# Optimization experiments

Measured on AMD Instinct MI355X. Metric: run time of the kernel, lower is better.

Reference implementation:

```python
import jax, jax.numpy as jnp
import numpy as np

B, N, C = 8, 4096, 768
H = 12            # num_heads
W = 16            # window_size
S = int(N ** 0.5) # 64, token grid side
HD = C // H       # head_dim = 64
WINDOWS = (S // W) ** 2  # 16
NW = W * W               # 256 tokens per window
SCALE = HD ** -0.5


def _window_perm():
    # same ordering as the torch loop: row-major over window blocks,
    # row-major within each window
    idxs = np.arange(N).reshape(S // W, W, S // W, W)
    perm = idxs.transpose(0, 2, 1, 3).reshape(-1)
    inv_perm = np.argsort(perm)
    return jnp.asarray(perm), jnp.asarray(inv_perm)


def setup_inputs() -> dict:
    key = jax.random.key(0)
    kx, kq, kp, kb = jax.random.split(key, 4)
    x = jax.random.normal(kx, (B, N, C), dtype=jnp.float32)
    # torch nn.Linear weights: [out, in]; qkv_bias=False
    qkv_w = jax.random.normal(kq, (3 * C, C), dtype=jnp.float32) * (C ** -0.5)
    proj_w = jax.random.normal(kp, (C, C), dtype=jnp.float32) * (C ** -0.5)
    proj_b = jax.random.normal(kb, (C,), dtype=jnp.float32) * 0.02
    return {"x": x, "qkv_w": qkv_w, "proj_w": proj_w, "proj_b": proj_b}


def reference(x, qkv_w, proj_w, proj_b):
    perm, inv_perm = _window_perm()
    xp = x[:, perm]                                   # [B, N, C] window-ordered
    qkv = xp @ qkv_w.T                                # [B, N, 3C]
    qkv = qkv.reshape(B, WINDOWS, NW, 3, H, HD)
    qkv = jnp.transpose(qkv, (3, 0, 1, 4, 2, 5))      # [3, B, Wn, H, NW, HD]
    q, k, v = qkv[0], qkv[1], qkv[2]
    attn = jnp.einsum('bwhnd,bwhmd->bwhnm', q, k) * SCALE
    attn = jax.nn.softmax(attn, axis=-1)
    out = jnp.einsum('bwhnm,bwhmd->bwhnd', attn, v)   # [B, Wn, H, NW, HD]
    out = jnp.transpose(out, (0, 1, 3, 2, 4)).reshape(B, N, C)
    out = out[:, inv_perm]                            # scatter back to grid order
    return out @ proj_w.T + proj_b
```

## Files before the change

kernel.cpp:

```cpp
#include <hip/hip_runtime.h>
#include <hip/hip_bf16.h>


using short8  = __attribute__((ext_vector_type(8))) short;
using short4v = __attribute__((ext_vector_type(4))) short;
using floatx4 = __attribute__((ext_vector_type(4))) float;

#define B_    8
#define N_    4096
#define C_    768
#define H_    12
#define HD_   64
#define NW_   256
#define SCALE_ 0.125f
#define QKV_PLANE ((size_t)25165824)

__device__ __forceinline__ float bf2f(unsigned short u) {
  union { unsigned int i; float f; } c; c.i = ((unsigned int)u) << 16; return c.f;
}
__device__ __forceinline__ unsigned short f2bf(float f) {
  unsigned int u = __float_as_uint(f);
  u += 0x7fffu + ((u >> 16) & 1u);
  return (unsigned short)(u >> 16);
}
__device__ __forceinline__ short4v f4bf(floatx4 f) {
  short4v s;
  s[0] = (short)f2bf(f[0]); s[1] = (short)f2bf(f[1]);
  s[2] = (short)f2bf(f[2]); s[3] = (short)f2bf(f[3]);
  return s;
}
__device__ __forceinline__ int perm_n(int w, int t) {
  int rb = w >> 2, cb = w & 3, ri = t >> 4, ci = t & 15;
  return ((rb << 4) + ri) * 64 + (cb << 4) + ci;
}
__device__ __forceinline__ void glds16(const unsigned short* g, short* l) {
  __builtin_amdgcn_global_load_lds(
      (const __attribute__((address_space(1))) unsigned int*)g,
      (__attribute__((address_space(3))) unsigned int*)l, 16, 0, 0);
}

__global__ __launch_bounds__(192) void conv_x(
    const float* __restrict__ x, unsigned short* __restrict__ xb) {
  int row = blockIdx.x;
  int b = row >> 12, p = row & 4095;
  int n = perm_n(p >> 8, p & 255);
  const float* src = x + ((size_t)(b << 12) + (size_t)n) * C_;
  unsigned short* dst = xb + (size_t)row * C_;
  int c = threadIdx.x << 2;
  *(short4v*)(dst + c) = f4bf(*(const floatx4*)(src + c));
}

__global__ __launch_bounds__(192) void conv_w(
    const float* __restrict__ qw, const float* __restrict__ pw,
    unsigned short* __restrict__ wq, unsigned short* __restrict__ wp) {
  int row = blockIdx.x;
  const float* src; unsigned short* dst;
  if (row < 2304) { src = qw + (size_t)row * C_; dst = wq + (size_t)row * C_; }
  else { src = pw + (size_t)(row - 2304) * C_; dst = wp + (size_t)(row - 2304) * C_; }
  int c = threadIdx.x << 2;
  *(short4v*)(dst + c) = f4bf(*(const floatx4*)(src + c));
}

#define GEMM_CORE(Aptr, Bptr)                                                  \
  __shared__ short As[128 * 32];                                               \
  __shared__ short Bs[128 * 32];                                               \
  const int tid  = threadIdx.x;                                                \
  const int id0  = (int)(blockIdx.y * gridDim.x + blockIdx.x);                 \
  const int cpx  = (int)(gridDim.x * gridDim.y) >> 3;                          \
  const int swz  = (id0 & 7) * cpx + (id0 >> 3);                               \
  const int bm   = swz & 255;                                                  \
  const int bn   = swz >> 8;                                                   \
  const int wave = tid >> 6, lane = tid & 63;                                  \
  const int wm   = wave >> 1, wn = wave & 1;                                   \
  const int l15  = lane & 15, quad = lane >> 4;                                \
  const int srow = tid >> 2, skof = (tid & 3) << 3;                            \
  const unsigned short* ga0 = (Aptr) + (size_t)(bm * 128 + srow) * C_ + skof;  \
  const unsigned short* ga1 = ga0 + (size_t)64 * C_;                           \
  const unsigned short* gb0 = (Bptr) + (size_t)(bn * 128 + srow) * C_ + skof;  \
  const unsigned short* gb1 = gb0 + (size_t)64 * C_;                           \
  short* la0 = As + tid * 8;                                                   \
  short* la1 = As + 2048 + tid * 8;                                            \
  short* lb0 = Bs + tid * 8;                                                   \
  short* lb1 = Bs + 2048 + tid * 8;                                            \
  floatx4 acc[4][4];                                                           \
  _Pragma("unroll") for (int i = 0; i < 4; i++)                                \
      _Pragma("unroll") for (int j = 0; j < 4; j++)                            \
          acc[i][j] = {0.f, 0.f, 0.f, 0.f};                                    \
  for (int k0 = 0; k0 < C_; k0 += 32) {                                        \
    glds16(ga0 + k0, la0);                                                     \
    glds16(ga1 + k0, la1);                                                     \
    glds16(gb0 + k0, lb0);                                                     \
    glds16(gb1 + k0, lb1);                                                     \
    __syncthreads();                                                           \
    short8 af[4], bfr[4];                                                      \
    _Pragma("unroll") for (int mi = 0; mi < 4; mi++)                           \
        af[mi] = *(const short8*)&As[(wm * 64 + mi * 16 + l15) * 32 + quad * 8];\
    _Pragma("unroll") for (int ni = 0; ni < 4; ni++)                           \
        bfr[ni] = *(const short8*)&Bs[(wn * 64 + ni * 16 + l15) * 32 + quad * 8];\
    _Pragma("unroll") for (int mi = 0; mi < 4; mi++)                           \
        _Pragma("unroll") for (int ni = 0; ni < 4; ni++)                       \
            acc[mi][ni] = __builtin_amdgcn_mfma_f32_16x16x32_bf16(             \
                af[mi], bfr[ni], acc[mi][ni], 0, 0, 0);                        \
    __syncthreads();                                                           \
  }

__global__ __launch_bounds__(256) void qkv_gemm_bf(
    const unsigned short* __restrict__ a,
    const unsigned short* __restrict__ w,
    unsigned short* __restrict__ qkv) {
  GEMM_CORE(a, w)
  const int which = (bn * 128) / 768;
  const int jbase = bn * 128 - which * 768;
  unsigned short* dst = qkv + (size_t)which * QKV_PLANE;
#pragma unroll
  for (int mi = 0; mi < 4; mi++) {
#pragma unroll
    for (int r = 0; r < 4; r++) {
      int mg = bm * 128 + wm * 64 + mi * 16 + quad * 4 + r;
      int b = mg >> 12, p = mg & 4095;
      int wdx = p >> 8, t = p & 255;
      size_t base = (size_t)((b * 16 + wdx) * 12) * (NW_ * HD_) + (size_t)t * HD_;
#pragma unroll
      for (int ni = 0; ni < 4; ni++) {
        int jj = jbase + wn * 64 + ni * 16 + l15;
        int h = jj >> 6, d = jj & 63;
        dst[base + (size_t)h * (NW_ * HD_) + d] = f2bf(acc[mi][ni][r]);
      }
    }
  }
}

__global__ __launch_bounds__(256) void proj_gemm_bf(
    const unsigned short* __restrict__ a,
    const unsigned short* __restrict__ w,
    const float* __restrict__ bias,
    float* __restrict__ out) {
  GEMM_CORE(a, w)
#pragma unroll
  for (int mi = 0; mi < 4; mi++) {
#pragma unroll
    for (int r = 0; r < 4; r++) {
      int mg = bm * 128 + wm * 64 + mi * 16 + quad * 4 + r;
      size_t rowb = (size_t)mg * C_;
#pragma unroll
      for (int ni = 0; ni < 4; ni++) {
        int jj = bn * 128 + wn * 64 + ni * 16 + l15;
        out[rowb + jj] = acc[mi][ni][r] + bias[jj];
      }
    }
  }
}

__global__ __launch_bounds__(512, 2) void attn_mfma(
    const unsigned short* __restrict__ qkv,
    unsigned short* __restrict__ attn_out) {
  const int bwh = blockIdx.x;
  const int tid = threadIdx.x;
  const int wv = tid >> 6, lane = tid & 63;
  const int l15 = lane & 15, quad = lane >> 4;
  const size_t off = (size_t)bwh * (NW_ * HD_);
  const unsigned short* qb = qkv + off;
  const unsigned short* kb = qkv + QKV_PLANE + off;
  const unsigned short* vb = qkv + 2 * QKV_PLANE + off;

  __shared__ short Ks[64 * 72];
  __shared__ short Vt[64 * 72];
  __shared__ short Ps[8][16 * 72];

  short8 bq[2][2];
#pragma unroll
  for (int c = 0; c < 2; c++) {
    int mc = wv + 8 * c;
#pragma unroll
    for (int kc = 0; kc < 2; kc++)
      bq[c][kc] = *(const short8*)(qb + (mc * 16 + l15) * 64 + kc * 32 + quad * 8);
  }

  floatx4 O[2][4];
#pragma unroll
  for (int c = 0; c < 2; c++)
#pragma unroll
    for (int dt = 0; dt < 4; dt++) O[c][dt] = {0.f, 0.f, 0.f, 0.f};
  float m_run[2] = {-1e30f, -1e30f};
  float l_run[2] = {0.f, 0.f};

  const int sr = tid >> 3;
  const int sc = (tid & 7) << 3;

  for (int t = 0; t < 4; t++) {
    __syncthreads();
    {
      short8 kk8 = *(const short8*)(kb + (t * 64 + sr) * 64 + sc);
      *(short8*)&Ks[sr * 72 + sc] = kk8;
      short8 vv8 = *(const short8*)(vb + (t * 64 + sr) * 64 + sc);
#pragma unroll
      for (int j = 0; j < 8; j++) Vt[(sc + j) * 72 + sr] = vv8[j];
    }
    __syncthreads();

#pragma unroll
    for (int c = 0; c < 2; c++) {
      floatx4 st[4];
#pragma unroll
      for (int nt = 0; nt < 4; nt++) {
        short8 ak0 = *(const short8*)&Ks[(nt * 16 + l15) * 72 + quad * 8];
        short8 ak1 = *(const short8*)&Ks[(nt * 16 + l15) * 72 + 32 + quad * 8];
        floatx4 z = {0.f, 0.f, 0.f, 0.f};
        z = __builtin_amdgcn_mfma_f32_16x16x32_bf16(ak0, bq[c][0], z, 0, 0, 0);
        z = __builtin_amdgcn_mfma_f32_16x16x32_bf16(ak1, bq[c][1], z, 0, 0, 0);
        st[nt] = z;
      }
      float s[16];
      float cmax = -1e30f;
#pragma unroll
      for (int nt = 0; nt < 4; nt++)
#pragma unroll
        for (int r = 0; r < 4; r++) {
          float v = st[nt][r] * SCALE_;
          s[nt * 4 + r] = v;
          cmax = fmaxf(cmax, v);
        }
      cmax = fmaxf(cmax, __shfl_xor(cmax, 16));
      cmax = fmaxf(cmax, __shfl_xor(cmax, 32));
      float nm = fmaxf(m_run[c], cmax);
      float alpha = __expf(m_run[c] - nm);
      m_run[c] = nm;
      float psum = 0.f;
#pragma unroll
      for (int j = 0; j < 16; j++) {
        float p = __expf(s[j] - nm);
        s[j] = p;
        psum += p;
      }
      psum += __shfl_xor(psum, 16);
      psum += __shfl_xor(psum, 32);
      l_run[c] = l_run[c] * alpha + psum;
#pragma unroll
      for (int nt = 0; nt < 4; nt++) {
        short4v pv;
        pv[0] = (short)f2bf(s[nt * 4 + 0]);
        pv[1] = (short)f2bf(s[nt * 4 + 1]);
        pv[2] = (short)f2bf(s[nt * 4 + 2]);
        pv[3] = (short)f2bf(s[nt * 4 + 3]);
        *(short4v*)&Ps[wv][l15 * 72 + nt * 16 + quad * 4] = pv;
      }
      float ar[4];
#pragma unroll
      for (int r = 0; r < 4; r++) ar[r] = __shfl(alpha, quad * 4 + r);
#pragma unroll
      for (int dt = 0; dt < 4; dt++)
#pragma unroll
        for (int r = 0; r < 4; r++) O[c][dt][r] *= ar[r];
#pragma unroll
      for (int kc = 0; kc < 2; kc++) {
        short8 ap = *(const short8*)&Ps[wv][l15 * 72 + kc * 32 + quad * 8];
#pragma unroll
        for (int dt = 0; dt < 4; dt++) {
          short8 bv = *(const short8*)&Vt[(dt * 16 + l15) * 72 + kc * 32 + quad * 8];
          O[c][dt] = __builtin_amdgcn_mfma_f32_16x16x32_bf16(ap, bv, O[c][dt], 0, 0, 0);
        }
      }
    }
  }

  int h = bwh % 12, bw = bwh / 12;
  int b = bw >> 4, wdx = bw & 15;
#pragma unroll
  for (int c = 0; c < 2; c++) {
    float linv = 1.f / l_run[c];
    float lr[4];
#pragma unroll
    for (int r = 0; r < 4; r++) lr[r] = __shfl(linv, quad * 4 + r);
    int mc = wv + 8 * c;
#pragma unroll
    for (int r = 0; r < 4; r++) {
      int q = mc * 16 + quad * 4 + r;
      int n = perm_n(wdx, q);
      unsigned short* op = attn_out + ((size_t)(b * N_ + n)) * C_ + h * HD_;
#pragma unroll
      for (int dt = 0; dt < 4; dt++)
        op[dt * 16 + l15] = f2bf(O[c][dt][r] * lr[r]);
    }
  }
}

__global__ __launch_bounds__(256) void qkv_gemm_f32(
    const float* __restrict__ x,
    const float* __restrict__ w,
    unsigned short* __restrict__ qkv) {
  __shared__ short As[128 * 40];
  __shared__ short Bs[128 * 40];
  const int tid  = threadIdx.x;
  const int bm   = blockIdx.x;
  const int bn   = blockIdx.y;
  const int wave = tid >> 6, lane = tid & 63;
  const int wm   = wave >> 1, wn = wave & 1;
  const int l15  = lane & 15, quad = lane >> 4;
  const int colf  = (tid & 7) << 2;
  const int rbase = tid >> 3;
  size_t aoff[4], boff[4];
#pragma unroll
  for (int i = 0; i < 4; i++) {
    int r = rbase + 32 * i;
    int mg = bm * 128 + r;
    int b = mg >> 12, p = mg & 4095;
    int n = perm_n(p >> 8, p & 255);
    aoff[i] = ((size_t)(b << 12) + (size_t)n) * C_;
    boff[i] = (size_t)(bn * 128 + r) * C_;
  }
  floatx4 acc[4][4];
#pragma unroll
  for (int i = 0; i < 4; i++)
#pragma unroll
    for (int j = 0; j < 4; j++) acc[i][j] = {0.f, 0.f, 0.f, 0.f};
  for (int k0 = 0; k0 < C_; k0 += 32) {
#pragma unroll
    for (int i = 0; i < 4; i++) {
      int r = rbase + 32 * i;
      *(short4v*)&As[r * 40 + colf] = f4bf(*(const floatx4*)(x + aoff[i] + k0 + colf));
      *(short4v*)&Bs[r * 40 + colf] = f4bf(*(const floatx4*)(w + boff[i] + k0 + colf));
    }
    __syncthreads();
    short8 af[4], bfr[4];
#pragma unroll
    for (int mi = 0; mi < 4; mi++)
      af[mi] = *(const short8*)&As[(wm * 64 + mi * 16 + l15) * 40 + quad * 8];
#pragma unroll
    for (int ni = 0; ni < 4; ni++)
      bfr[ni] = *(const short8*)&Bs[(wn * 64 + ni * 16 + l15) * 40 + quad * 8];
#pragma unroll
    for (int mi = 0; mi < 4; mi++)
#pragma unroll
      for (int ni = 0; ni < 4; ni++)
        acc[mi][ni] = __builtin_amdgcn_mfma_f32_16x16x32_bf16(
            af[mi], bfr[ni], acc[mi][ni], 0, 0, 0);
    __syncthreads();
  }
  const int which = (bn * 128) / 768;
  const int jbase = bn * 128 - which * 768;
  unsigned short* dst = qkv + (size_t)which * QKV_PLANE;
#pragma unroll
  for (int mi = 0; mi < 4; mi++) {
#pragma unroll
    for (int r = 0; r < 4; r++) {
      int mg = bm * 128 + wm * 64 + mi * 16 + quad * 4 + r;
      int b = mg >> 12, p = mg & 4095;
      int wdx = p >> 8, t = p & 255;
      size_t base = (size_t)((b * 16 + wdx) * 12) * (NW_ * HD_) + (size_t)t * HD_;
#pragma unroll
      for (int ni = 0; ni < 4; ni++) {
        int jj = jbase + wn * 64 + ni * 16 + l15;
        int h = jj >> 6, d = jj & 63;
        dst[base + (size_t)h * (NW_ * HD_) + d] = f2bf(acc[mi][ni][r]);
      }
    }
  }
}

__global__ __launch_bounds__(256) void proj_gemm_f32(
    const unsigned short* __restrict__ a,
    const float* __restrict__ w,
    const float* __restrict__ bias,
    float* __restrict__ out) {
  __shared__ short As[128 * 40];
  __shared__ short Bs[128 * 40];
  const int tid  = threadIdx.x;
  const int bm   = blockIdx.x;
  const int bn   = blockIdx.y;
  const int wave = tid >> 6, lane = tid & 63;
  const int wm   = wave >> 1, wn = wave & 1;
  const int l15  = lane & 15, quad = lane >> 4;
  const int c0 = tid, c1 = tid + 256;
  const int r0 = c0 >> 2, kc0 = (c0 & 3) << 3;
  const int r1 = c1 >> 2, kc1 = (c1 & 3) << 3;
  const size_t a0 = (size_t)(bm * 128 + r0) * C_;
  const size_t a1 = (size_t)(bm * 128 + r1) * C_;
  const int colf  = (tid & 7) << 2;
  const int rbase = tid >> 3;
  size_t boff[4];
#pragma unroll
  for (int i = 0; i < 4; i++)
    boff[i] = (size_t)(bn * 128 + rbase + 32 * i) * C_;
  floatx4 acc[4][4];
#pragma unroll
  for (int i = 0; i < 4; i++)
#pragma unroll
    for (int j = 0; j < 4; j++) acc[i][j] = {0.f, 0.f, 0.f, 0.f};
  for (int k0 = 0; k0 < C_; k0 += 32) {
    *(short8*)&As[r0 * 40 + kc0] = *(const short8*)(a + a0 + k0 + kc0);
    *(short8*)&As[r1 * 40 + kc1] = *(const short8*)(a + a1 + k0 + kc1);
#pragma unroll
    for (int i = 0; i < 4; i++) {
      int r = rbase + 32 * i;
      *(short4v*)&Bs[r * 40 + colf] = f4bf(*(const floatx4*)(w + boff[i] + k0 + colf));
    }
    __syncthreads();
    short8 af[4], bfr[4];
#pragma unroll
    for (int mi = 0; mi < 4; mi++)
      af[mi] = *(const short8*)&As[(wm * 64 + mi * 16 + l15) * 40 + quad * 8];
#pragma unroll
    for (int ni = 0; ni < 4; ni++)
      bfr[ni] = *(const short8*)&Bs[(wn * 64 + ni * 16 + l15) * 40 + quad * 8];
#pragma unroll
    for (int mi = 0; mi < 4; mi++)
#pragma unroll
      for (int ni = 0; ni < 4; ni++)
        acc[mi][ni] = __builtin_amdgcn_mfma_f32_16x16x32_bf16(
            af[mi], bfr[ni], acc[mi][ni], 0, 0, 0);
    __syncthreads();
  }
#pragma unroll
  for (int mi = 0; mi < 4; mi++) {
#pragma unroll
    for (int r = 0; r < 4; r++) {
      int mg = bm * 128 + wm * 64 + mi * 16 + quad * 4 + r;
      size_t rowb = (size_t)mg * C_;
#pragma unroll
      for (int ni = 0; ni < 4; ni++) {
        int jj = bn * 128 + wn * 64 + ni * 16 + l15;
        out[rowb + jj] = acc[mi][ni][r] + bias[jj];
      }
    }
  }
}

extern "C" void kernel_launch(void* const* d_in, const int* in_sizes, int n_in,
                              void* d_out, int out_size, void* d_ws, size_t ws_size,
                              hipStream_t stream) {
  const float* x  = (const float*)d_in[0];
  const float* qw = (const float*)d_in[1];
  const float* pw = (const float*)d_in[2];
  const float* pb = (const float*)d_in[3];
  float* out = (float*)d_out;
  unsigned short* ws = (unsigned short*)d_ws;

  unsigned short* xb       = ws;
  unsigned short* qkv_buf  = ws + QKV_PLANE;
  unsigned short* attn_buf = ws;
  unsigned short* wb_qkv   = ws + 4 * QKV_PLANE;
  unsigned short* wb_proj  = wb_qkv + (size_t)2304 * 768;

  const size_t need = (4 * QKV_PLANE + (size_t)2304 * 768 + (size_t)768 * 768) * 2;
  if (ws_size >= need) {
    conv_x<<<dim3(B_ * N_), dim3(192), 0, stream>>>(x, xb);
    conv_w<<<dim3(3072), dim3(192), 0, stream>>>(qw, pw, wb_qkv, wb_proj);
    qkv_gemm_bf<<<dim3(256, 18), dim3(256), 0, stream>>>(xb, wb_qkv, qkv_buf);
    attn_mfma<<<dim3(1536), dim3(512), 0, stream>>>(qkv_buf, attn_buf);
    proj_gemm_bf<<<dim3(256, 6), dim3(256), 0, stream>>>(attn_buf, wb_proj, pb, out);
  } else {
    qkv_gemm_f32<<<dim3(256, 18), dim3(256), 0, stream>>>(x, qw, qkv_buf);
    attn_mfma<<<dim3(1536), dim3(512), 0, stream>>>(qkv_buf, attn_buf);
    proj_gemm_f32<<<dim3(256, 6), dim3(256), 0, stream>>>(attn_buf, pw, pb, out);
  }
}
```

Before: 484.4 us.

## Rewrite bf16 GEMMs as 256x256 tiles with double-buffered LDS pipeline

Replaces the 128x128, single-buffered GEMM core used by the QKV and projection GEMMs with a 256x256-tile, 8-wave kernel. It uses 128 KB of double-buffered LDS, XOR-swizzled LDS addressing, and phased async global-to-LDS loads that overlap with MFMA work, with explicit barriers, waitcnt and setprio scheduling. The goal is to hide global load latency, raise data reuse per tile and avoid LDS bank conflicts in the GEMMs. The cost is a larger LDS footprint, fewer blocks in the grid and the removal of the L2-friendly block swizzle, plus fragile hand-tuned synchronization.

```diff
diff --git a/kernel.cpp b/kernel.cpp
--- a/kernel.cpp
+++ b/kernel.cpp
@@ -61,65 +61,113 @@
   *(short4v*)(dst + c) = f4bf(*(const floatx4*)(src + c));
 }
 
-#define GEMM_CORE(Aptr, Bptr)                                                  \
-  __shared__ short As[128 * 32];                                               \
-  __shared__ short Bs[128 * 32];                                               \
+#define LPA 0
+#define LPB 16384
+#define LQA 32768
+#define LQB 49152
+
+#define STAGE8(gp, ldsbase, ksk) {                                             \
+    int kc_ = (ksk) < C_ ? (ksk) : 0;                                          \
+    glds16((gp) + (size_t)arow * C_ + kc_ + (sgran << 3),                      \
+           L + (ldsbase) + tid * 8);                                           \
+    glds16((gp) + (size_t)(arow + 64) * C_ + kc_ + (sgran << 3),               \
+           L + (ldsbase) + 4096 + tid * 8);                                    \
+  }
+
+#define PH8(q, AB, BB, LOADB, STG_STMT, WV) {                                  \
+    if (LOADB) {                                                               \
+      _Pragma("unroll") for (int n = 0; n < 4; n++)                            \
+        _Pragma("unroll") for (int kk = 0; kk < 2; kk++)                       \
+          bq[n][kk] = *(const short8*)&L[(BB) + rdB + n * 1024 +               \
+                                          (((kk * 4 + quad) ^ swq) << 3)];     \
+    }                                                                          \
+    short8 a0k0 = *(const short8*)&L[(AB) + rdA + (2*(q))*1024 +               \
+                                      (((quad) ^ swq) << 3)];                  \
+    short8 a0k1 = *(const short8*)&L[(AB) + rdA + (2*(q))*1024 +               \
+                                      (((4 + quad) ^ swq) << 3)];              \
+    short8 a1k0 = *(const short8*)&L[(AB) + rdA + (2*(q)+1)*1024 +             \
+                                      (((quad) ^ swq) << 3)];                  \
+    short8 a1k1 = *(const short8*)&L[(AB) + rdA + (2*(q)+1)*1024 +             \
+                                      (((4 + quad) ^ swq) << 3)];              \
+    STG_STMT;                                                                  \
+    asm volatile("s_barrier" ::: "memory");                                    \
+    asm volatile("s_waitcnt lgkmcnt(0)" ::: "memory");                         \
+    __builtin_amdgcn_sched_barrier(0);                                         \
+    __builtin_amdgcn_s_setprio(1);                                             \
+    _Pragma("unroll") for (int n = 0; n < 4; n++) {                            \
+      acc[2*(q)][n]   = __builtin_amdgcn_mfma_f32_16x16x32_bf16(               \
+          a0k0, bq[n][0], acc[2*(q)][n], 0, 0, 0);                             \
+      acc[2*(q)+1][n] = __builtin_amdgcn_mfma_f32_16x16x32_bf16(               \
+          a1k0, bq[n][0], acc[2*(q)+1][n], 0, 0, 0);                           \
+      acc[2*(q)][n]   = __builtin_amdgcn_mfma_f32_16x16x32_bf16(               \
+          a0k1, bq[n][1], acc[2*(q)][n], 0, 0, 0);                             \
+      acc[2*(q)+1][n] = __builtin_amdgcn_mfma_f32_16x16x32_bf16(               \
+          a1k1, bq[n][1], acc[2*(q)+1][n], 0, 0, 0);                           \
+    }                                                                          \
+    __builtin_amdgcn_s_setprio(0);                                             \
+    if (WV) { asm volatile("s_waitcnt vmcnt(4)" ::: "memory"); }               \
+    asm volatile("s_barrier" ::: "memory");                                    \
+  }
+
+#define GEMM8_CORE(Aptr, Bptr)                                                 \
+  __shared__ short L[65536];                                                   \
   const int tid  = threadIdx.x;                                                \
-  const int id0  = (int)(blockIdx.y * gridDim.x + blockIdx.x);                 \
-  const int cpx  = (int)(gridDim.x * gridDim.y) >> 3;                          \
-  const int swz  = (id0 & 7) * cpx + (id0 >> 3);                               \
-  const int bm   = swz & 255;                                                  \
-  const int bn   = swz >> 8;                                                   \
+  const int bm   = blockIdx.x;                                                 \
+  const int bn   = blockIdx.y;                                                 \
   const int wave = tid >> 6, lane = tid & 63;                                  \
-  const int wm   = wave >> 1, wn = wave & 1;                                   \
+  const int wm   = wave >> 2, wn = wave & 3;                                   \
   const int l15  = lane & 15, quad = lane >> 4;                                \
-  const int srow = tid >> 2, skof = (tid & 3) << 3;                            \
-  const unsigned short* ga0 = (Aptr) + (size_t)(bm * 128 + srow) * C_ + skof;  \
-  const unsigned short* ga1 = ga0 + (size_t)64 * C_;                           \
-  const unsigned short* gb0 = (Bptr) + (size_t)(bn * 128 + srow) * C_ + skof;  \
-  const unsigned short* gb1 = gb0 + (size_t)64 * C_;                           \
-  short* la0 = As + tid * 8;                                                   \
-  short* la1 = As + 2048 + tid * 8;                                            \
-  short* lb0 = Bs + tid * 8;                                                   \
-  short* lb1 = Bs + 2048 + tid * 8;                                            \
-  floatx4 acc[4][4];                                                           \
-  _Pragma("unroll") for (int i = 0; i < 4; i++)                                \
+  const int swq  = l15 & 7;                                                    \
+  const int sgran = (tid & 7) ^ ((tid >> 3) & 7);                              \
+  const int arow  = tid >> 3;                                                  \
+  const unsigned short* gA = (Aptr) + (size_t)(bm * 256) * C_;                 \
+  const unsigned short* gB = (Bptr) + (size_t)(bn * 256) * C_;                 \
+  const unsigned short* gA1 = gA + (size_t)128 * C_;                           \
+  const unsigned short* gB1 = gB + (size_t)128 * C_;                           \
+  const int rdA = wm * 8192 + l15 * 64;                                        \
+  const int rdB = (wn >> 1) * 8192 + ((wn & 1) * 64 + l15) * 64;               \
+  floatx4 acc[8][4];                                                           \
+  short8 bq[4][2];                                                             \
+  _Pragma("unroll") for (int i = 0; i < 8; i++)                                \
       _Pragma("unroll") for (int j = 0; j < 4; j++)                            \
           acc[i][j] = {0.f, 0.f, 0.f, 0.f};                                    \
-  for (int k0 = 0; k0 < C_; k0 += 32) {                                        \
-    glds16(ga0 + k0, la0);                                                     \
-    glds16(ga1 + k0, la1);                                                     \
-    glds16(gb0 + k0, lb0);                                                     \
-    glds16(gb1 + k0, lb1);                                                     \
-    __syncthreads();                                                           \
-    short8 af[4], bfr[4];                                                      \
-    _Pragma("unroll") for (int mi = 0; mi < 4; mi++)                           \
-        af[mi] = *(const short8*)&As[(wm * 64 + mi * 16 + l15) * 32 + quad * 8];\
-    _Pragma("unroll") for (int ni = 0; ni < 4; ni++)                           \
-        bfr[ni] = *(const short8*)&Bs[(wn * 64 + ni * 16 + l15) * 32 + quad * 8];\
-    _Pragma("unroll") for (int mi = 0; mi < 4; mi++)                           \
-        _Pragma("unroll") for (int ni = 0; ni < 4; ni++)                       \
-            acc[mi][ni] = __builtin_amdgcn_mfma_f32_16x16x32_bf16(             \
-                af[mi], bfr[ni], acc[mi][ni], 0, 0, 0);                        \
-    __syncthreads();                                                           \
-  }
-
-__global__ __launch_bounds__(256) void qkv_gemm_bf(
+                           \
+  STAGE8(gA,  LPA,        0); STAGE8(gA1, LPA + 8192, 0);                      \
+  STAGE8(gB,  LPB,        0); STAGE8(gB1, LPB + 8192, 0);                      \
+  STAGE8(gB,  LQB,       64); STAGE8(gB1, LQB + 8192, 64);                     \
+  asm volatile("s_waitcnt vmcnt(4)" ::: "memory");                             \
+  asm volatile("s_barrier" ::: "memory");                                      \
+  for (int it = 0; it < 6; it++) {                                             \
+    const int t  = it * 2;                                                     \
+    const int kA1 = (t + 1) * 64;                                              \
+    const int kN2 = (t + 2) * 64;                                              \
+    const int kN3 = (t + 3) * 64;                                              \
+    PH8(0, LPA, LPB, 1, STAGE8(gA,  LQA,        kA1), 0)                       \
+    PH8(1, LPA, LPB, 0, STAGE8(gA1, LQA + 8192, kA1), 0)                       \
+    PH8(2, LPA, LPB, 0, STAGE8(gB,  LPB,        kN2), 0)                       \
+    PH8(3, LPA, LPB, 0, STAGE8(gB1, LPB + 8192, kN2), 1)                       \
+    PH8(0, LQA, LQB, 1, STAGE8(gA,  LPA,        kN2), 0)                       \
+    PH8(1, LQA, LQB, 0, STAGE8(gA1, LPA + 8192, kN2), 0)                       \
+    PH8(2, LQA, LQB, 0, STAGE8(gB,  LQB,        kN3), 0)                       \
+    PH8(3, LQA, LQB, 0, STAGE8(gB1, LQB + 8192, kN3), 1)                       \
+  }
+
+__global__ __launch_bounds__(512, 2) void qkv_gemm_bf8(
     const unsigned short* __restrict__ a,
     const unsigned short* __restrict__ w,
     unsigned short* __restrict__ qkv) {
-  GEMM_CORE(a, w)
-  const int which = (bn * 128) / 768;
-  const int jbase = bn * 128 - which * 768;
+  GEMM8_CORE(a, w)
+  const int which = bn / 3;
+  const int jbase = (bn - which * 3) * 256;
   unsigned short* dst = qkv + (size_t)which * QKV_PLANE;
 #pragma unroll
-  for (int mi = 0; mi < 4; mi++) {
+  for (int mi = 0; mi < 8; mi++) {
 #pragma unroll
     for (int r = 0; r < 4; r++) {
-      int mg = bm * 128 + wm * 64 + mi * 16 + quad * 4 + r;
+      int mg = bm * 256 + wm * 128 + mi * 16 + quad * 4 + r;
       int b = mg >> 12, p = mg & 4095;
-      int wdx = p >> 8, t = p & 255;
-      size_t base = (size_t)((b * 16 + wdx) * 12) * (NW_ * HD_) + (size_t)t * HD_;
+      int wdx = p >> 8, tt = p & 255;
+      size_t base = (size_t)((b * 16 + wdx) * 12) * (NW_ * HD_) + (size_t)tt * HD_;
 #pragma unroll
       for (int ni = 0; ni < 4; ni++) {
         int jj = jbase + wn * 64 + ni * 16 + l15;
@@ -128,27 +176,29 @@
       }
     }
   }
-}
-
-__global__ __launch_bounds__(256) void proj_gemm_bf(
+  asm volatile("s_waitcnt vmcnt(0)" ::: "memory");
+}
+
+__global__ __launch_bounds__(512, 2) void proj_gemm_bf8(
     const unsigned short* __restrict__ a,
     const unsigned short* __restrict__ w,
     const float* __restrict__ bias,
     float* __restrict__ out) {
-  GEMM_CORE(a, w)
-#pragma unroll
-  for (int mi = 0; mi < 4; mi++) {
+  GEMM8_CORE(a, w)
+#pragma unroll
+  for (int mi = 0; mi < 8; mi++) {
 #pragma unroll
     for (int r = 0; r < 4; r++) {
-      int mg = bm * 128 + wm * 64 + mi * 16 + quad * 4 + r;
+      int mg = bm * 256 + wm * 128 + mi * 16 + quad * 4 + r;
       size_t rowb = (size_t)mg * C_;
 #pragma unroll
       for (int ni = 0; ni < 4; ni++) {
-        int jj = bn * 128 + wn * 64 + ni * 16 + l15;
+        int jj = bn * 256 + wn * 64 + ni * 16 + l15;
         out[rowb + jj] = acc[mi][ni][r] + bias[jj];
       }
     }
   }
+  asm volatile("s_waitcnt vmcnt(0)" ::: "memory");
 }
 
 __global__ __launch_bounds__(512, 2) void attn_mfma(
@@ -445,9 +495,9 @@
   if (ws_size >= need) {
     conv_x<<<dim3(B_ * N_), dim3(192), 0, stream>>>(x, xb);
     conv_w<<<dim3(3072), dim3(192), 0, stream>>>(qw, pw, wb_qkv, wb_proj);
-    qkv_gemm_bf<<<dim3(256, 18), dim3(256), 0, stream>>>(xb, wb_qkv, qkv_buf);
+    qkv_gemm_bf8<<<dim3(128, 9), dim3(512), 0, stream>>>(xb, wb_qkv, qkv_buf);
     attn_mfma<<<dim3(1536), dim3(512), 0, stream>>>(qkv_buf, attn_buf);
-    proj_gemm_bf<<<dim3(256, 6), dim3(256), 0, stream>>>(attn_buf, wb_proj, pb, out);
+    proj_gemm_bf8<<<dim3(128, 3), dim3(512), 0, stream>>>(attn_buf, wb_proj, pb, out);
   } else {
     qkv_gemm_f32<<<dim3(256, 18), dim3(256), 0, stream>>>(x, qw, qkv_buf);
     attn_mfma<<<dim3(1536), dim3(512), 0, stream>>>(qkv_buf, attn_buf);
```

Result: faster. 439.0 us (-9.4%).
